# Performance work log

Measured on AMD Instinct MI355X. Metric: run time of the kernel, lower is better.

## Reference

```python
import jax, jax.numpy as jnp
import numpy as np

H = 16  # num heads
ROPE_BASE = 10000.0

def _rope(t):
    # t: [B, T, H, D]; half-split (rotate_half / LLaMA-style) rotary embedding
    B, T, nH, D = t.shape
    half = D // 2
    inv_freq = 1.0 / (ROPE_BASE ** (jnp.arange(0, half, dtype=jnp.float32) / half))
    ang = jnp.arange(T, dtype=jnp.float32)[:, None] * inv_freq[None, :]  # [T, half]
    cos = jnp.cos(ang)[None, :, None, :]  # [1,T,1,half]
    sin = jnp.sin(ang)[None, :, None, :]
    t1, t2 = t[..., :half], t[..., half:]
    return jnp.concatenate([t1 * cos - t2 * sin, t2 * cos + t1 * sin], axis=-1)

def setup_inputs() -> dict:
    key = jax.random.key(0)
    ks = jax.random.split(key, 5)
    B, T, C = 2, 2048, 1024
    s = 1.0 / np.sqrt(C)
    return {
        "x": jax.random.normal(ks[0], (B, T, C), jnp.float32),
        "Wqkv": jax.random.normal(ks[1], (C, 3 * C), jnp.float32) * s,
        "bqkv": jnp.zeros((3 * C,), jnp.float32),
        "Wout": jax.random.normal(ks[2], (C, C), jnp.float32) * s,
        "bout": jnp.zeros((C,), jnp.float32),
    }

def reference(x, Wqkv, bqkv, Wout, bout):
    B, T, C = x.shape
    D = C // H
    qkv = (x @ Wqkv + bqkv).reshape(B, T, 3, H, D)
    q, k, v = qkv[:, :, 0], qkv[:, :, 1], qkv[:, :, 2]  # [B,T,H,D]
    q = _rope(q)
    k = _rope(k)
    scale = 1.0 / jnp.sqrt(jnp.asarray(D, x.dtype))
    scores = jnp.einsum('bqhd,bkhd->bhqk', q, k) * scale
    probs = jax.nn.softmax(scores, axis=-1)
    attn = jnp.einsum('bhqk,bkhd->bqhd', probs, v).reshape(B, T, C)
    return attn @ Wout + bout
```

## Files before the change

### kernel.cpp

```cpp
#include <hip/hip_runtime.h>

typedef float f32x4 __attribute__((ext_vector_type(4)));
typedef short bf16x8 __attribute__((ext_vector_type(8)));

#define DEV __device__ __forceinline__

DEV unsigned short f2bf(float x) {
  union { float f; unsigned u; } v; v.f = x;
  unsigned r = v.u + 0x7fffu + ((v.u >> 16) & 1u);
  return (unsigned short)(r >> 16);
}
DEV float bf2f(unsigned short h) {
  union { unsigned u; float f; } v; v.u = ((unsigned)h) << 16;
  return v.f;
}

#if defined(__has_builtin)
# if __has_builtin(__builtin_amdgcn_global_load_lds)
#  define HAVE_GLL 1
# endif
# if __has_builtin(__builtin_amdgcn_exp2f)
#  define EXP2(x) __builtin_amdgcn_exp2f(x)
# else
#  define EXP2(x) exp2f(x)
# endif
#else
# define EXP2(x) exp2f(x)
#endif

DEV unsigned pk_bf16_trunc(float a, float b) {
  return __builtin_amdgcn_perm(__float_as_uint(b), __float_as_uint(a), 0x07060302u);
}

DEV void g2l16(const unsigned short* g, unsigned short* l) {
#ifdef HAVE_GLL
  __builtin_amdgcn_global_load_lds((const __attribute__((address_space(1))) void*)g,
                                   (__attribute__((address_space(3))) void*)l, 16, 0, 0);
#else
  *(uint4*)l = *(const uint4*)g;
#endif
}

__global__ void rope_tab(float* cosb, float* sinb) {
  int i = blockIdx.x * 256 + threadIdx.x;
  int t = i >> 5, d = i & 31;
  float invf = (float)(1.0 / pow(10000.0, (double)d / 32.0));
  float ang = (float)t * invf;
  cosb[i] = (float)cos((double)ang);
  sinb[i] = (float)sin((double)ang);
}

__global__ void castA(const float* __restrict__ in, unsigned short* __restrict__ out) {
  int i = blockIdx.x * 256 + threadIdx.x;
  f32x4 v = ((const f32x4*)in)[i];
  ushort4 o;
  o.x = f2bf(v[0]); o.y = f2bf(v[1]); o.z = f2bf(v[2]); o.w = f2bf(v[3]);
  ((ushort4*)out)[i] = o;
}

__global__ __launch_bounds__(256) void transW(const float* __restrict__ W,
                                              unsigned short* __restrict__ Wt, int N) {
  __shared__ float t[64 * 65];
  int k0 = blockIdx.x * 64, n0 = blockIdx.y * 64;
  for (int idx = threadIdx.x; idx < 4096; idx += 256) {
    int kl = idx >> 6, nl = idx & 63;
    t[kl * 65 + nl] = W[(size_t)(k0 + kl) * N + n0 + nl];
  }
  __syncthreads();
  for (int idx = threadIdx.x; idx < 4096; idx += 256) {
    int nl = idx >> 6, kl = idx & 63;
    Wt[(size_t)(n0 + nl) * 1024 + k0 + kl] = f2bf(t[kl * 65 + nl]);
  }
}

template <typename OutT>
__global__ __launch_bounds__(256, 2) void gemm128(
    const unsigned short* __restrict__ A, const unsigned short* __restrict__ Bt,
    const float* __restrict__ bias, OutT* __restrict__ C, int M, int N, int K) {
  __shared__ alignas(16) unsigned short As[128 * 64];
  __shared__ alignas(16) unsigned short Bs[128 * 64];
  const int tid = threadIdx.x;
  const int lane = tid & 63, wave = tid >> 6;
  const int l15 = lane & 15, quad = lane >> 4;
  const int m0 = blockIdx.y * 128, n0 = blockIdx.x * 128;
  const int wm = (wave & 1) * 64, wn = (wave >> 1) * 64;

  f32x4 acc[4][4];
#pragma unroll
  for (int i = 0; i < 4; i++)
#pragma unroll
    for (int j = 0; j < 4; j++)
#pragma unroll
      for (int r = 0; r < 4; r++) acc[i][j][r] = 0.f;

  const int nkt = K >> 6;
  for (int kt = 0; kt < nkt; ++kt) {
    __syncthreads();
#pragma unroll
    for (int i = 0; i < 4; ++i) {
      int u = i * 256 + tid;
      int row = u >> 3;
      int kcg = (u & 7) ^ (row & 7);
      g2l16(A  + (size_t)(m0 + row) * K + (kt << 6) + (kcg << 3), As + u * 8);
      g2l16(Bt + (size_t)(n0 + row) * K + (kt << 6) + (kcg << 3), Bs + u * 8);
    }
    __syncthreads();
#pragma unroll
    for (int ks = 0; ks < 2; ++ks) {
      const int kc = ks * 4 + quad;
      bf16x8 af[4], bfr[4];
#pragma unroll
      for (int t = 0; t < 4; ++t) {
        int mrow = wm + t * 16 + l15;
        af[t] = *(const bf16x8*)(As + (mrow * 8 + (kc ^ (mrow & 7))) * 8);
        int nrow = wn + t * 16 + l15;
        bfr[t] = *(const bf16x8*)(Bs + (nrow * 8 + (kc ^ (nrow & 7))) * 8);
      }
#pragma unroll
      for (int mt = 0; mt < 4; ++mt)
#pragma unroll
        for (int nt = 0; nt < 4; ++nt)
          acc[mt][nt] = __builtin_amdgcn_mfma_f32_16x16x32_bf16(af[mt], bfr[nt], acc[mt][nt], 0, 0, 0);
    }
  }
#pragma unroll
  for (int mt = 0; mt < 4; ++mt)
#pragma unroll
    for (int nt = 0; nt < 4; ++nt) {
      int col = n0 + wn + nt * 16 + l15;
      int rowb = m0 + wm + mt * 16 + quad * 4;
      float bb = bias[col];
#pragma unroll
      for (int r = 0; r < 4; ++r) {
        float v = acc[mt][nt][r] + bb;
        if constexpr (sizeof(OutT) == 2)
          C[(size_t)(rowb + r) * N + col] = (OutT)f2bf(v);
        else
          C[(size_t)(rowb + r) * N + col] = (OutT)v;
      }
    }
}

__global__ __launch_bounds__(256, 2) void gemm64(
    const unsigned short* __restrict__ A, const unsigned short* __restrict__ Bt,
    const float* __restrict__ bias, float* __restrict__ C, int M, int N, int K) {
  __shared__ alignas(16) unsigned short As[64 * 64];
  __shared__ alignas(16) unsigned short Bs[128 * 64];
  const int tid = threadIdx.x;
  const int lane = tid & 63, wave = tid >> 6;
  const int l15 = lane & 15, quad = lane >> 4;
  const int m0 = blockIdx.y * 64, n0 = blockIdx.x * 128;
  const int wm = (wave & 1) * 32, wn = (wave >> 1) * 64;

  f32x4 acc[2][4];
#pragma unroll
  for (int i = 0; i < 2; i++)
#pragma unroll
    for (int j = 0; j < 4; j++)
#pragma unroll
      for (int r = 0; r < 4; r++) acc[i][j][r] = 0.f;

  const int nkt = K >> 6;
  for (int kt = 0; kt < nkt; ++kt) {
    __syncthreads();
#pragma unroll
    for (int i = 0; i < 2; ++i) {
      int u = i * 256 + tid;
      int row = u >> 3;
      int kcg = (u & 7) ^ (row & 7);
      g2l16(A + (size_t)(m0 + row) * K + (kt << 6) + (kcg << 3), As + u * 8);
    }
#pragma unroll
    for (int i = 0; i < 4; ++i) {
      int u = i * 256 + tid;
      int row = u >> 3;
      int kcg = (u & 7) ^ (row & 7);
      g2l16(Bt + (size_t)(n0 + row) * K + (kt << 6) + (kcg << 3), Bs + u * 8);
    }
    __syncthreads();
#pragma unroll
    for (int ks = 0; ks < 2; ++ks) {
      const int kc = ks * 4 + quad;
      bf16x8 af[2], bfr[4];
#pragma unroll
      for (int t = 0; t < 2; ++t) {
        int mrow = wm + t * 16 + l15;
        af[t] = *(const bf16x8*)(As + (mrow * 8 + (kc ^ (mrow & 7))) * 8);
      }
#pragma unroll
      for (int t = 0; t < 4; ++t) {
        int nrow = wn + t * 16 + l15;
        bfr[t] = *(const bf16x8*)(Bs + (nrow * 8 + (kc ^ (nrow & 7))) * 8);
      }
#pragma unroll
      for (int mt = 0; mt < 2; ++mt)
#pragma unroll
        for (int nt = 0; nt < 4; ++nt)
          acc[mt][nt] = __builtin_amdgcn_mfma_f32_16x16x32_bf16(af[mt], bfr[nt], acc[mt][nt], 0, 0, 0);
    }
  }
#pragma unroll
  for (int mt = 0; mt < 2; ++mt)
#pragma unroll
    for (int nt = 0; nt < 4; ++nt) {
      int col = n0 + wn + nt * 16 + l15;
      int rowb = m0 + wm + mt * 16 + quad * 4;
      float bb = bias[col];
#pragma unroll
      for (int r = 0; r < 4; ++r)
        C[(size_t)(rowb + r) * N + col] = acc[mt][nt][r] + bb;
    }
}

#define QSCALE 0.180336880f
__global__ __launch_bounds__(256) void repack(const unsigned short* __restrict__ qkv,
                                              const float* __restrict__ cosb,
                                              const float* __restrict__ sinb,
                                              unsigned short* __restrict__ Qb,
                                              unsigned short* __restrict__ Kb,
                                              unsigned short* __restrict__ Vt) {
  __shared__ float vl[64 * 65];
  int bh = blockIdx.x, b = bh >> 4, h = bh & 15;
  int t0 = blockIdx.y * 64;
  for (int idx = threadIdx.x; idx < 4096; idx += 256) {
    int tl = idx >> 6, dd = idx & 63;
    int t = t0 + tl;
    const unsigned short* row = qkv + (size_t)(b * 2048 + t) * 3072;
    int dr = dd & 31;
    float c = cosb[t * 32 + dr], s = sinb[t * 32 + dr];
    const unsigned short* qp = row + h * 64;
    const unsigned short* kp = row + 1024 + h * 64;
    float qv, kv;
    if (dd < 32) { qv = bf2f(qp[dd]) * c - bf2f(qp[dd + 32]) * s;
                   kv = bf2f(kp[dd]) * c - bf2f(kp[dd + 32]) * s; }
    else         { qv = bf2f(qp[dd]) * c + bf2f(qp[dd - 32]) * s;
                   kv = bf2f(kp[dd]) * c + bf2f(kp[dd - 32]) * s; }
    Qb[((size_t)bh * 2048 + t) * 64 + dd] = f2bf(QSCALE * qv);
    Kb[((size_t)bh * 2048 + t) * 64 + dd] = f2bf(kv);
    vl[tl * 65 + dd] = bf2f(row[2048 + h * 64 + dd]);
  }
  __syncthreads();
  for (int idx = threadIdx.x; idx < 4096; idx += 256) {
    int dl = idx >> 6, tl = idx & 63;
    Vt[((size_t)bh * 64 + dl) * 2048 + t0 + tl] = f2bf(vl[tl * 65 + dl]);
  }
}

__global__ __launch_bounds__(256, 2) void flash_attn(const unsigned short* __restrict__ Qb,
                                                     const unsigned short* __restrict__ Kb,
                                                     const unsigned short* __restrict__ Vt,
                                                     unsigned short* __restrict__ O) {
  __shared__ alignas(16) unsigned short Ks[64 * 64];
  __shared__ alignas(16) unsigned short Vs[64 * 64];
  __shared__ alignas(16) unsigned short Ps[4 * 32 * 64];
  const int tid = threadIdx.x, lane = tid & 63, wave = tid >> 6;
  const int l15 = lane & 15, quad = lane >> 4;
  const int bh = blockIdx.x, qb = blockIdx.y;
  const int q0 = qb * 128 + wave * 32;
  const size_t qbase = ((size_t)bh * 2048 + q0) * 64;
  bf16x8 qf[2][2];
#pragma unroll
  for (int ks = 0; ks < 2; ++ks)
#pragma unroll
    for (int qg = 0; qg < 2; ++qg)
      qf[ks][qg] = *(const bf16x8*)(Qb + qbase + (qg * 16 + l15) * 64 + ks * 32 + quad * 8);

  f32x4 o[2][4];
#pragma unroll
  for (int qg = 0; qg < 2; qg++)
#pragma unroll
    for (int nt = 0; nt < 4; nt++)
#pragma unroll
      for (int r = 0; r < 4; r++) o[qg][nt][r] = 0.f;
  float li[2] = {0.f, 0.f};
  const f32x4 negb = {-12.f, -12.f, -12.f, -12.f};
  unsigned short* Pw = Ps + wave * (32 * 64);

  for (int kb = 0; kb < 32; ++kb) {
    __syncthreads();
#pragma unroll
    for (int i = 0; i < 2; ++i) {
      int u = i * 256 + tid;
      int row = u >> 3;
      int cg = (u & 7) ^ (row & 7);
      g2l16(Kb + ((size_t)bh * 2048 + kb * 64 + row) * 64 + cg * 8, Ks + u * 8);
      g2l16(Vt + ((size_t)bh * 64 + row) * 2048 + kb * 64 + cg * 8, Vs + u * 8);
    }
    __syncthreads();
    f32x4 sacc[2][4];
#pragma unroll
    for (int ks = 0; ks < 2; ++ks) {
      const int kc = ks * 4 + quad;
#pragma unroll
      for (int mt = 0; mt < 4; ++mt) {
        int key = mt * 16 + l15;
        bf16x8 kf = *(const bf16x8*)(Ks + (key * 8 + (kc ^ (key & 7))) * 8);
        if (ks == 0) {
          sacc[0][mt] = __builtin_amdgcn_mfma_f32_16x16x32_bf16(kf, qf[0][0], negb, 0, 0, 0);
          sacc[1][mt] = __builtin_amdgcn_mfma_f32_16x16x32_bf16(kf, qf[0][1], negb, 0, 0, 0);
        } else {
          sacc[0][mt] = __builtin_amdgcn_mfma_f32_16x16x32_bf16(kf, qf[1][0], sacc[0][mt], 0, 0, 0);
          sacc[1][mt] = __builtin_amdgcn_mfma_f32_16x16x32_bf16(kf, qf[1][1], sacc[1][mt], 0, 0, 0);
        }
      }
    }
#pragma unroll
    for (int qg = 0; qg < 2; ++qg) {
      int row = qg * 16 + l15;
      float psum = 0.f;
#pragma unroll
      for (int mt = 0; mt < 4; ++mt) {
        float p0 = EXP2(sacc[qg][mt][0]);
        float p1 = EXP2(sacc[qg][mt][1]);
        float p2 = EXP2(sacc[qg][mt][2]);
        float p3 = EXP2(sacc[qg][mt][3]);
        psum += (p0 + p1) + (p2 + p3);
        uint2 w;
        w.x = pk_bf16_trunc(p0, p1);
        w.y = pk_bf16_trunc(p2, p3);
        int kg = mt * 2 + (quad >> 1);
        *(uint2*)(Pw + (row * 8 + (kg ^ (row & 7))) * 8 + (quad & 1) * 4) = w;
      }
      li[qg] += psum;
    }
#pragma unroll
    for (int ks = 0; ks < 2; ++ks) {
      const int kc = ks * 4 + quad;
      bf16x8 pf0 = *(const bf16x8*)(Pw + ((l15) * 8 + (kc ^ (l15 & 7))) * 8);
      bf16x8 pf1 = *(const bf16x8*)(Pw + ((16 + l15) * 8 + (kc ^ (l15 & 7))) * 8);
#pragma unroll
      for (int nt = 0; nt < 4; ++nt) {
        int dd = nt * 16 + l15;
        bf16x8 vf = *(const bf16x8*)(Vs + (dd * 8 + (kc ^ (dd & 7))) * 8);
        o[0][nt] = __builtin_amdgcn_mfma_f32_16x16x32_bf16(pf0, vf, o[0][nt], 0, 0, 0);
        o[1][nt] = __builtin_amdgcn_mfma_f32_16x16x32_bf16(pf1, vf, o[1][nt], 0, 0, 0);
      }
    }
  }
  const int b = bh >> 4, h = bh & 15;
#pragma unroll
  for (int qg = 0; qg < 2; ++qg) {
    li[qg] += __shfl_xor(li[qg], 16);
    li[qg] += __shfl_xor(li[qg], 32);
#pragma unroll
    for (int r = 0; r < 4; ++r) {
      float lr = __shfl(li[qg], quad * 4 + r);
      float inv = 1.001953125f / lr;
      int row = b * 2048 + q0 + qg * 16 + quad * 4 + r;
#pragma unroll
      for (int nt = 0; nt < 4; ++nt)
        O[(size_t)row * 1024 + h * 64 + nt * 16 + l15] = f2bf(o[qg][nt][r] * inv);
    }
  }
}

extern "C" void kernel_launch(void* const* d_in, const int* in_sizes, int n_in,
                              void* d_out, int out_size, void* d_ws, size_t ws_size,
                              hipStream_t stream) {
  const float* x    = (const float*)d_in[0];
  const float* Wqkv = (const float*)d_in[1];
  const float* bqkv = (const float*)d_in[2];
  const float* Wout = (const float*)d_in[3];
  const float* bout = (const float*)d_in[4];
  float* out = (float*)d_out;
  char* ws = (char*)d_ws;
  float*          COS  = (float*)(ws + 0);
  float*          SIN  = (float*)(ws + 262144);
  unsigned short* A1   = (unsigned short*)(ws + 524288);
  unsigned short* W1t  = (unsigned short*)(ws + 8912896);
  unsigned short* W2t  = (unsigned short*)(ws + 15204352);
  unsigned short* QKVb = (unsigned short*)(ws + 17301504);
  unsigned short* QB   = (unsigned short*)(ws + 42467328);
  unsigned short* KB   = (unsigned short*)(ws + 50855936);
  unsigned short* VT   = (unsigned short*)(ws + 59244544);
  unsigned short* A2   = (unsigned short*)(ws + 67633152);

  rope_tab<<<256, 256, 0, stream>>>(COS, SIN);
  castA<<<4096, 256, 0, stream>>>(x, A1);
  transW<<<dim3(16, 48), 256, 0, stream>>>(Wqkv, W1t, 3072);
  transW<<<dim3(16, 16), 256, 0, stream>>>(Wout, W2t, 1024);
  gemm128<unsigned short><<<dim3(24, 32), 256, 0, stream>>>(A1, W1t, bqkv, QKVb, 4096, 3072, 1024);
  repack<<<dim3(32, 32), 256, 0, stream>>>(QKVb, COS, SIN, QB, KB, VT);
  flash_attn<<<dim3(32, 16), 256, 0, stream>>>(QB, KB, VT, A2);
  gemm64<<<dim3(8, 64), 256, 0, stream>>>(A2, W2t, bout, out, 4096, 1024, 1024);
}
```

Baseline: 200.8 us.

## Fuse RoPE and V transpose into QKV GEMM epilogue; keep P in registers

The separate repack kernel is removed. The QKV GEMM epilogue now applies bias, RoPE and the Q scale, writes Q/K into a combined row-major buffer and writes V already transposed, which saves a full round trip of the QKV tensor through memory and one launch. Flash attention now computes P·V as V^T·P with 16x16x16 MFMAs so the probabilities stay in registers instead of going through LDS. Blocks drop to 128 threads so there are twice as many of them. Q/K loads are now strided through the 2048-wide QK buffer, and the epilogue V stores are narrow scattered writes.

```diff
diff --git a/kernel.cpp b/kernel.cpp
--- a/kernel.cpp
+++ b/kernel.cpp
@@ -2,6 +2,7 @@
 
 typedef float f32x4 __attribute__((ext_vector_type(4)));
 typedef short bf16x8 __attribute__((ext_vector_type(8)));
+typedef short bf16x4 __attribute__((ext_vector_type(4)));
 
 #define DEV __device__ __forceinline__
 
@@ -31,6 +32,9 @@
 DEV unsigned pk_bf16_trunc(float a, float b) {
   return __builtin_amdgcn_perm(__float_as_uint(b), __float_as_uint(a), 0x07060302u);
 }
+DEV unsigned pk_bf16_rnd(float a, float b) {
+  return ((unsigned)f2bf(b) << 16) | f2bf(a);
+}
 
 DEV void g2l16(const unsigned short* g, unsigned short* l) {
 #ifdef HAVE_GLL
@@ -41,6 +45,15 @@
 #endif
 }
 
+DEV f32x4 mfma16x16x16(bf16x4 a, bf16x4 b, f32x4 c) {
+#if defined(__has_builtin) && __has_builtin(__builtin_amdgcn_mfma_f32_16x16x16bf16_1k)
+  return __builtin_amdgcn_mfma_f32_16x16x16bf16_1k(a, b, c, 0, 0, 0);
+#else
+  asm volatile("v_mfma_f32_16x16x16_bf16 %0, %1, %2, %0" : "+v"(c) : "v"(a), "v"(b));
+  return c;
+#endif
+}
+
 __global__ void rope_tab(float* cosb, float* sinb) {
   int i = blockIdx.x * 256 + threadIdx.x;
   int t = i >> 5, d = i & 31;
@@ -73,10 +86,13 @@
   }
 }
 
-template <typename OutT>
-__global__ __launch_bounds__(256, 2) void gemm128(
+#define QSCALE 0.180336880f
+__global__ __launch_bounds__(256, 2) void gemm_qkv(
     const unsigned short* __restrict__ A, const unsigned short* __restrict__ Bt,
-    const float* __restrict__ bias, OutT* __restrict__ C, int M, int N, int K) {
+    const float* __restrict__ bias, const float* __restrict__ cosb,
+    const float* __restrict__ sinb, unsigned short* __restrict__ QK,
+    unsigned short* __restrict__ Vt) {
+  const int K = 1024;
   __shared__ alignas(16) unsigned short As[128 * 64];
   __shared__ alignas(16) unsigned short Bs[128 * 64];
   const int tid = threadIdx.x;
@@ -93,8 +109,7 @@
 #pragma unroll
       for (int r = 0; r < 4; r++) acc[i][j][r] = 0.f;
 
-  const int nkt = K >> 6;
-  for (int kt = 0; kt < nkt; ++kt) {
+  for (int kt = 0; kt < 16; ++kt) {
     __syncthreads();
 #pragma unroll
     for (int i = 0; i < 4; ++i) {
@@ -123,22 +138,45 @@
           acc[mt][nt] = __builtin_amdgcn_mfma_f32_16x16x32_bf16(af[mt], bfr[nt], acc[mt][nt], 0, 0, 0);
     }
   }
-#pragma unroll
-  for (int mt = 0; mt < 4; ++mt)
-#pragma unroll
-    for (int nt = 0; nt < 4; ++nt) {
-      int col = n0 + wn + nt * 16 + l15;
-      int rowb = m0 + wm + mt * 16 + quad * 4;
-      float bb = bias[col];
+  const int headcol = n0 + wn;
+  const int b = m0 >> 11;
+  float bb[4];
+#pragma unroll
+  for (int nt = 0; nt < 4; ++nt) bb[nt] = bias[headcol + nt * 16 + l15];
+
+  if (headcol < 2048) {
+    const float scale = (headcol < 1024) ? QSCALE : 1.f;
+#pragma unroll
+    for (int mt = 0; mt < 4; ++mt) {
 #pragma unroll
       for (int r = 0; r < 4; ++r) {
-        float v = acc[mt][nt][r] + bb;
-        if constexpr (sizeof(OutT) == 2)
-          C[(size_t)(rowb + r) * N + col] = (OutT)f2bf(v);
-        else
-          C[(size_t)(rowb + r) * N + col] = (OutT)v;
-      }
-    }
+        int row = m0 + wm + mt * 16 + quad * 4 + r;
+        int t = row & 2047;
+#pragma unroll
+        for (int nt = 0; nt < 2; ++nt) {
+          int d = nt * 16 + l15;
+          float c = cosb[t * 32 + d], s = sinb[t * 32 + d];
+          float v1 = acc[mt][nt][r] + bb[nt];
+          float v2 = acc[mt][nt + 2][r] + bb[nt + 2];
+          QK[(size_t)row * 2048 + headcol + d]      = f2bf((v1 * c - v2 * s) * scale);
+          QK[(size_t)row * 2048 + headcol + d + 32] = f2bf((v2 * c + v1 * s) * scale);
+        }
+      }
+    }
+  } else {
+    const int hv = (headcol - 2048) >> 6;
+    const int t0 = (m0 + wm) & 2047;
+#pragma unroll
+    for (int mt = 0; mt < 4; ++mt)
+#pragma unroll
+      for (int nt = 0; nt < 4; ++nt) {
+        int d = nt * 16 + l15;
+        uint2 w;
+        w.x = pk_bf16_rnd(acc[mt][nt][0] + bb[nt], acc[mt][nt][1] + bb[nt]);
+        w.y = pk_bf16_rnd(acc[mt][nt][2] + bb[nt], acc[mt][nt][3] + bb[nt]);
+        *(uint2*)(Vt + ((size_t)((b * 16 + hv) * 64 + d)) * 2048 + t0 + mt * 16 + quad * 4) = w;
+      }
+  }
 }
 
 __global__ __launch_bounds__(256, 2) void gemm64(
@@ -205,66 +243,30 @@
     for (int nt = 0; nt < 4; ++nt) {
       int col = n0 + wn + nt * 16 + l15;
       int rowb = m0 + wm + mt * 16 + quad * 4;
-      float bb = bias[col];
+      float b = bias[col];
 #pragma unroll
       for (int r = 0; r < 4; ++r)
-        C[(size_t)(rowb + r) * N + col] = acc[mt][nt][r] + bb;
-    }
-}
-
-#define QSCALE 0.180336880f
-__global__ __launch_bounds__(256) void repack(const unsigned short* __restrict__ qkv,
-                                              const float* __restrict__ cosb,
-                                              const float* __restrict__ sinb,
-                                              unsigned short* __restrict__ Qb,
-                                              unsigned short* __restrict__ Kb,
-                                              unsigned short* __restrict__ Vt) {
-  __shared__ float vl[64 * 65];
-  int bh = blockIdx.x, b = bh >> 4, h = bh & 15;
-  int t0 = blockIdx.y * 64;
-  for (int idx = threadIdx.x; idx < 4096; idx += 256) {
-    int tl = idx >> 6, dd = idx & 63;
-    int t = t0 + tl;
-    const unsigned short* row = qkv + (size_t)(b * 2048 + t) * 3072;
-    int dr = dd & 31;
-    float c = cosb[t * 32 + dr], s = sinb[t * 32 + dr];
-    const unsigned short* qp = row + h * 64;
-    const unsigned short* kp = row + 1024 + h * 64;
-    float qv, kv;
-    if (dd < 32) { qv = bf2f(qp[dd]) * c - bf2f(qp[dd + 32]) * s;
-                   kv = bf2f(kp[dd]) * c - bf2f(kp[dd + 32]) * s; }
-    else         { qv = bf2f(qp[dd]) * c + bf2f(qp[dd - 32]) * s;
-                   kv = bf2f(kp[dd]) * c + bf2f(kp[dd - 32]) * s; }
-    Qb[((size_t)bh * 2048 + t) * 64 + dd] = f2bf(QSCALE * qv);
-    Kb[((size_t)bh * 2048 + t) * 64 + dd] = f2bf(kv);
-    vl[tl * 65 + dd] = bf2f(row[2048 + h * 64 + dd]);
-  }
-  __syncthreads();
-  for (int idx = threadIdx.x; idx < 4096; idx += 256) {
-    int dl = idx >> 6, tl = idx & 63;
-    Vt[((size_t)bh * 64 + dl) * 2048 + t0 + tl] = f2bf(vl[tl * 65 + dl]);
-  }
-}
-
-__global__ __launch_bounds__(256, 2) void flash_attn(const unsigned short* __restrict__ Qb,
-                                                     const unsigned short* __restrict__ Kb,
+        C[(size_t)(rowb + r) * N + col] = acc[mt][nt][r] + b;
+    }
+}
+
+__global__ __launch_bounds__(128, 2) void flash_attn(const unsigned short* __restrict__ QK,
                                                      const unsigned short* __restrict__ Vt,
                                                      unsigned short* __restrict__ O) {
   __shared__ alignas(16) unsigned short Ks[64 * 64];
   __shared__ alignas(16) unsigned short Vs[64 * 64];
-  __shared__ alignas(16) unsigned short Ps[4 * 32 * 64];
   const int tid = threadIdx.x, lane = tid & 63, wave = tid >> 6;
   const int l15 = lane & 15, quad = lane >> 4;
   const int bh = blockIdx.x, qb = blockIdx.y;
-  const int q0 = qb * 128 + wave * 32;
-  const size_t qbase = ((size_t)bh * 2048 + q0) * 64;
+  const int b = bh >> 4, h = bh & 15;
+  const int q0 = qb * 64 + wave * 32;
   bf16x8 qf[2][2];
 #pragma unroll
   for (int ks = 0; ks < 2; ++ks)
 #pragma unroll
     for (int qg = 0; qg < 2; ++qg)
-      qf[ks][qg] = *(const bf16x8*)(Qb + qbase + (qg * 16 + l15) * 64 + ks * 32 + quad * 8);
-
+      qf[ks][qg] = *(const bf16x8*)(QK + (size_t)(b * 2048 + q0 + qg * 16 + l15) * 2048 +
+                                    h * 64 + ks * 32 + quad * 8);
   f32x4 o[2][4];
 #pragma unroll
   for (int qg = 0; qg < 2; qg++)
@@ -274,16 +276,15 @@
       for (int r = 0; r < 4; r++) o[qg][nt][r] = 0.f;
   float li[2] = {0.f, 0.f};
   const f32x4 negb = {-12.f, -12.f, -12.f, -12.f};
-  unsigned short* Pw = Ps + wave * (32 * 64);
 
   for (int kb = 0; kb < 32; ++kb) {
     __syncthreads();
 #pragma unroll
-    for (int i = 0; i < 2; ++i) {
-      int u = i * 256 + tid;
+    for (int i = 0; i < 4; ++i) {
+      int u = i * 128 + tid;
       int row = u >> 3;
       int cg = (u & 7) ^ (row & 7);
-      g2l16(Kb + ((size_t)bh * 2048 + kb * 64 + row) * 64 + cg * 8, Ks + u * 8);
+      g2l16(QK + (size_t)(b * 2048 + kb * 64 + row) * 2048 + 1024 + h * 64 + cg * 8, Ks + u * 8);
       g2l16(Vt + ((size_t)bh * 64 + row) * 2048 + kb * 64 + cg * 8, Vs + u * 8);
     }
     __syncthreads();
@@ -304,9 +305,18 @@
         }
       }
     }
+    bf16x4 vf[4][4];
+#pragma unroll
+    for (int nt = 0; nt < 4; ++nt)
+#pragma unroll
+      for (int mt = 0; mt < 4; ++mt) {
+        int dd = nt * 16 + l15;
+        int cg = mt * 2 + (quad >> 1);
+        vf[nt][mt] = *(const bf16x4*)(Vs + (dd * 8 + (cg ^ (dd & 7))) * 8 + (quad & 1) * 4);
+      }
 #pragma unroll
     for (int qg = 0; qg < 2; ++qg) {
-      int row = qg * 16 + l15;
+      bf16x4 pf[4];
       float psum = 0.f;
 #pragma unroll
       for (int mt = 0; mt < 4; ++mt) {
@@ -315,41 +325,31 @@
         float p2 = EXP2(sacc[qg][mt][2]);
         float p3 = EXP2(sacc[qg][mt][3]);
         psum += (p0 + p1) + (p2 + p3);
-        uint2 w;
-        w.x = pk_bf16_trunc(p0, p1);
-        w.y = pk_bf16_trunc(p2, p3);
-        int kg = mt * 2 + (quad >> 1);
-        *(uint2*)(Pw + (row * 8 + (kg ^ (row & 7))) * 8 + (quad & 1) * 4) = w;
+        union { uint2 u; bf16x4 v; } cc;
+        cc.u.x = pk_bf16_trunc(p0, p1);
+        cc.u.y = pk_bf16_trunc(p2, p3);
+        pf[mt] = cc.v;
       }
       li[qg] += psum;
-    }
-#pragma unroll
-    for (int ks = 0; ks < 2; ++ks) {
-      const int kc = ks * 4 + quad;
-      bf16x8 pf0 = *(const bf16x8*)(Pw + ((l15) * 8 + (kc ^ (l15 & 7))) * 8);
-      bf16x8 pf1 = *(const bf16x8*)(Pw + ((16 + l15) * 8 + (kc ^ (l15 & 7))) * 8);
-#pragma unroll
-      for (int nt = 0; nt < 4; ++nt) {
-        int dd = nt * 16 + l15;
-        bf16x8 vf = *(const bf16x8*)(Vs + (dd * 8 + (kc ^ (dd & 7))) * 8);
-        o[0][nt] = __builtin_amdgcn_mfma_f32_16x16x32_bf16(pf0, vf, o[0][nt], 0, 0, 0);
-        o[1][nt] = __builtin_amdgcn_mfma_f32_16x16x32_bf16(pf1, vf, o[1][nt], 0, 0, 0);
-      }
-    }
-  }
-  const int b = bh >> 4, h = bh & 15;
+#pragma unroll
+      for (int nt = 0; nt < 4; ++nt)
+#pragma unroll
+        for (int mt = 0; mt < 4; ++mt)
+          o[qg][nt] = mfma16x16x16(vf[nt][mt], pf[mt], o[qg][nt]);
+    }
+  }
 #pragma unroll
   for (int qg = 0; qg < 2; ++qg) {
     li[qg] += __shfl_xor(li[qg], 16);
     li[qg] += __shfl_xor(li[qg], 32);
-#pragma unroll
-    for (int r = 0; r < 4; ++r) {
-      float lr = __shfl(li[qg], quad * 4 + r);
-      float inv = 1.001953125f / lr;
-      int row = b * 2048 + q0 + qg * 16 + quad * 4 + r;
-#pragma unroll
-      for (int nt = 0; nt < 4; ++nt)
-        O[(size_t)row * 1024 + h * 64 + nt * 16 + l15] = f2bf(o[qg][nt][r] * inv);
+    float inv = 1.001953125f / li[qg];
+    size_t rowb = (size_t)(b * 2048 + q0 + qg * 16 + l15) * 1024 + h * 64;
+#pragma unroll
+    for (int nt = 0; nt < 4; ++nt) {
+      uint2 w;
+      w.x = pk_bf16_rnd(o[qg][nt][0] * inv, o[qg][nt][1] * inv);
+      w.y = pk_bf16_rnd(o[qg][nt][2] * inv, o[qg][nt][3] * inv);
+      *(uint2*)(O + rowb + nt * 16 + quad * 4) = w;
     }
   }
 }
@@ -369,18 +369,15 @@
   unsigned short* A1   = (unsigned short*)(ws + 524288);
   unsigned short* W1t  = (unsigned short*)(ws + 8912896);
   unsigned short* W2t  = (unsigned short*)(ws + 15204352);
-  unsigned short* QKVb = (unsigned short*)(ws + 17301504);
-  unsigned short* QB   = (unsigned short*)(ws + 42467328);
-  unsigned short* KB   = (unsigned short*)(ws + 50855936);
-  unsigned short* VT   = (unsigned short*)(ws + 59244544);
-  unsigned short* A2   = (unsigned short*)(ws + 67633152);
+  unsigned short* QK   = (unsigned short*)(ws + 17301504);
+  unsigned short* VT   = (unsigned short*)(ws + 34078720);
+  unsigned short* A2   = (unsigned short*)(ws + 42467328);
 
   rope_tab<<<256, 256, 0, stream>>>(COS, SIN);
   castA<<<4096, 256, 0, stream>>>(x, A1);
   transW<<<dim3(16, 48), 256, 0, stream>>>(Wqkv, W1t, 3072);
   transW<<<dim3(16, 16), 256, 0, stream>>>(Wout, W2t, 1024);
-  gemm128<unsigned short><<<dim3(24, 32), 256, 0, stream>>>(A1, W1t, bqkv, QKVb, 4096, 3072, 1024);
-  repack<<<dim3(32, 32), 256, 0, stream>>>(QKVb, COS, SIN, QB, KB, VT);
-  flash_attn<<<dim3(32, 16), 256, 0, stream>>>(QB, KB, VT, A2);
+  gemm_qkv<<<dim3(24, 32), 256, 0, stream>>>(A1, W1t, bqkv, COS, SIN, QK, VT);
+  flash_attn<<<dim3(32, 32), 128, 0, stream>>>(QK, VT, A2);
   gemm64<<<dim3(8, 64), 256, 0, stream>>>(A2, W2t, bout, out, 4096, 1024, 1024);
 }
```

Result: faster. 191.5 us (-4.6%).
